# Kernel tuning notes

Hardware: AMD Instinct MI355X
Metric: run time of the kernel (lower is better)

The kernel has to match this reference:

```python
import jax, jax.numpy as jnp
import numpy as np

B, N, C = 4, 8192, 512
H, Dh, G, R = 8, 64, 64, 2  # heads, dim_head, slice_num, mlp_ratio
EPS_LN = 1e-5
EPS_NORM = 1e-5


def _ln(x, g, b):
    m = jnp.mean(x, axis=-1, keepdims=True)
    v = jnp.var(x, axis=-1, keepdims=True)
    return (x - m) * jax.lax.rsqrt(v + EPS_LN) * g + b


def setup_inputs() -> dict:
    key = jax.random.key(0)
    ks = jax.random.split(key, 16)
    r = lambda k, shp: jax.random.normal(k, shp, jnp.float32) * 0.02
    inner = H * Dh
    return {
        "fx": jax.random.normal(ks[0], (B, N, C), jnp.float32),
        "ln1_g": jnp.ones((C,), jnp.float32), "ln1_b": jnp.zeros((C,), jnp.float32),
        "Wx": r(ks[1], (C, inner)), "bx": jnp.zeros((inner,), jnp.float32),
        "Wfx": r(ks[2], (C, inner)), "bfx": jnp.zeros((inner,), jnp.float32),
        "Wslice": r(ks[3], (Dh, G)), "bslice": jnp.zeros((G,), jnp.float32),
        "temperature": jnp.full((1, H, 1, 1), 0.5, jnp.float32),
        "Wq": r(ks[4], (Dh, Dh)), "Wk": r(ks[5], (Dh, Dh)), "Wv": r(ks[6], (Dh, Dh)),
        "Wout": r(ks[7], (inner, C)), "bout": jnp.zeros((C,), jnp.float32),
        "tln_g": jnp.ones((Dh,), jnp.float32), "tln_b": jnp.zeros((Dh,), jnp.float32),
        "Wm1": r(ks[8], (Dh, R * Dh)), "bm1": jnp.zeros((R * Dh,), jnp.float32),
        "Wm2": r(ks[9], (R * Dh, Dh)), "bm2": jnp.zeros((Dh,), jnp.float32),
    }


def reference(fx, ln1_g, ln1_b, Wx, bx, Wfx, bfx, Wslice, bslice, temperature,
              Wq, Wk, Wv, Wout, bout, tln_g, tln_b, Wm1, bm1, Wm2, bm2):
    fx_norm = _ln(fx, ln1_g, ln1_b)                          # [B,N,C]
    # _forward_slice: project to per-head mid features
    x_mid = (fx_norm @ Wx + bx).reshape(B, N, H, Dh).transpose(0, 2, 1, 3)   # [B,H,N,Dh]
    fx_mid = (fx_norm @ Wfx + bfx).reshape(B, N, H, Dh).transpose(0, 2, 1, 3)
    # _project_token: soft slice assignment + weighted pooling into G tokens
    logits = jnp.einsum('bhnd,dg->bhng', x_mid, Wslice) + bslice
    slice_w = jax.nn.softmax(logits / temperature, axis=-1)  # [B,H,N,G]
    slice_norm = jnp.sum(slice_w, axis=2)                    # [B,H,G]
    slice_tok = jnp.einsum('bhnd,bhng->bhgd', fx_mid, slice_w) / (slice_norm[..., None] + EPS_NORM)
    # attention over the small token set (G tokens)
    q = slice_tok @ Wq
    k = slice_tok @ Wk
    v = slice_tok @ Wv
    scale = Dh ** -0.5
    attn = jax.nn.softmax(jnp.einsum('bhgd,bhpd->bhgp', q, k) * scale, axis=-1)
    out_tok = jnp.einsum('bhgp,bhpd->bhgd', attn, v) + slice_tok
    # token MLP with residual
    h = _ln(out_tok, tln_g, tln_b)
    h = jax.nn.gelu(h @ Wm1 + bm1, approximate=False) @ Wm2 + bm2
    tokens = h + out_tok                                     # [B,H,G,Dh]
    # _deslice: weighted scatter back to N points, merge heads, out projection
    out_x = jnp.einsum('bhgd,bhng->bhnd', tokens, slice_w)
    out_x = out_x.transpose(0, 2, 1, 3).reshape(B, N, H * Dh)
    out = out_x @ Wout + bout
    return out + fx_norm
```

## Files before the change

kernel.cpp:

```cpp
#include <hip/hip_runtime.h>
#include <math.h>

#define B_ 4
#define N_ 8192
#define C_ 512
#define H_ 8
#define M_ (B_ * N_)

typedef __attribute__((ext_vector_type(8))) short bf16x8;
typedef __attribute__((ext_vector_type(4))) float f32x4;
typedef __attribute__((ext_vector_type(8))) unsigned short u16x8;
typedef __attribute__((ext_vector_type(4))) unsigned short u16x4;

__device__ __forceinline__ float b2f(unsigned short u) {
  union { unsigned int i; float f; } v;
  v.i = ((unsigned int)u) << 16;
  return v.f;
}
__device__ __forceinline__ unsigned short f2b(float f) {
  union { float f; unsigned int i; } v;
  v.f = f;
  unsigned int r = v.i + 0x7fff + ((v.i >> 16) & 1);
  return (unsigned short)(r >> 16);
}
__device__ __forceinline__ void gl_lds16(const void* g, void* l) {
  __builtin_amdgcn_global_load_lds(
      (const __attribute__((address_space(1))) unsigned int*)g,
      (__attribute__((address_space(3))) unsigned int*)l, 16, 0, 0);
}

__global__ __launch_bounds__(256) void ln_bf16(
    const float* __restrict__ x, const float* __restrict__ gam,
    const float* __restrict__ bet, unsigned short* __restrict__ y) {
  int wave = threadIdx.x >> 6, lane = threadIdx.x & 63;
  int row = (blockIdx.x << 2) + wave;
  const float4* xr = (const float4*)(x + (size_t)row * C_);
  float4 v0 = xr[lane], v1 = xr[lane + 64];
  float s = v0.x + v0.y + v0.z + v0.w + v1.x + v1.y + v1.z + v1.w;
  float q = v0.x * v0.x + v0.y * v0.y + v0.z * v0.z + v0.w * v0.w +
            v1.x * v1.x + v1.y * v1.y + v1.z * v1.z + v1.w * v1.w;
#pragma unroll
  for (int off = 32; off; off >>= 1) {
    s += __shfl_xor(s, off);
    q += __shfl_xor(q, off);
  }
  float mean = s * (1.0f / C_);
  float var = q * (1.0f / C_) - mean * mean;
  float rstd = rsqrtf(var + 1e-5f);
  const float4* gr = (const float4*)gam;
  const float4* br = (const float4*)bet;
  float4 g0 = gr[lane], g1 = gr[lane + 64];
  float4 b0 = br[lane], b1 = br[lane + 64];
  u16x4 oa, ob;
  oa.x = f2b((v0.x - mean) * rstd * g0.x + b0.x);
  oa.y = f2b((v0.y - mean) * rstd * g0.y + b0.y);
  oa.z = f2b((v0.z - mean) * rstd * g0.z + b0.z);
  oa.w = f2b((v0.w - mean) * rstd * g0.w + b0.w);
  ob.x = f2b((v1.x - mean) * rstd * g1.x + b1.x);
  ob.y = f2b((v1.y - mean) * rstd * g1.y + b1.y);
  ob.z = f2b((v1.z - mean) * rstd * g1.z + b1.z);
  ob.w = f2b((v1.w - mean) * rstd * g1.w + b1.w);
  unsigned short* yr = y + (size_t)row * C_;
  *(u16x4*)(yr + (lane << 2)) = oa;
  *(u16x4*)(yr + 256 + (lane << 2)) = ob;
}

__global__ __launch_bounds__(256) void prep_all(
    const float* __restrict__ Wx, const float* __restrict__ Wfx,
    const float* __restrict__ Wout, const float* __restrict__ Wsl,
    const float* __restrict__ Wq, const float* __restrict__ Wk,
    const float* __restrict__ Wv, const float* __restrict__ Wm1,
    const float* __restrict__ Wm2, unsigned short* __restrict__ WtX,
    unsigned short* __restrict__ WtF, unsigned short* __restrict__ WtO,
    unsigned short* __restrict__ wsf, unsigned short* __restrict__ wfr) {
  __shared__ float tile[64][65];
  int blk = blockIdx.x, t = threadIdx.x;
  if (blk < 192) {
    int which = blk >> 6, sub = blk & 63;
    const float* W = (which == 0) ? Wx : (which == 1) ? Wfx : Wout;
    unsigned short* Wt = (which == 0) ? WtX : (which == 1) ? WtF : WtO;
    int r0 = (sub >> 3) << 6, c0 = (sub & 7) << 6;
    int lr = t >> 4, lc = (t & 15) << 2;
#pragma unroll
    for (int p = 0; p < 4; p++) {
      float4 v = *(const float4*)(W + (size_t)(r0 + lr + p * 16) * 512 + c0 + lc);
      tile[lr + p * 16][lc + 0] = v.x;
      tile[lr + p * 16][lc + 1] = v.y;
      tile[lr + p * 16][lc + 2] = v.z;
      tile[lr + p * 16][lc + 3] = v.w;
    }
    __syncthreads();
    int on = t >> 2, ok = (t & 3) << 4;
    unsigned short tmp[16];
#pragma unroll
    for (int j = 0; j < 16; j++) tmp[j] = f2b(tile[ok + j][on]);
    unsigned short* op = Wt + (size_t)(c0 + on) * 512 + r0 + ok;
#pragma unroll
    for (int j4 = 0; j4 < 4; j4++)
      *(u16x4*)(op + (j4 << 2)) = *(u16x4*)(tmp + (j4 << 2));
  } else {
#pragma unroll
    for (int i = 0; i < 2; i++) {
      int idx = t + i * 256;
      int f = idx >> 6, l = idx & 63;
      int gt = f >> 1, ks = f & 1;
      int g = (gt << 4) + (l & 15);
      int d0 = (ks << 5) + ((l >> 4) << 3);
      unsigned short v[8];
#pragma unroll
      for (int jj = 0; jj < 8; jj++) v[jj] = f2b(Wsl[(size_t)(d0 + jj) * 64 + g]);
      *(u16x4*)(wsf + idx * 8) = *(u16x4*)v;
      *(u16x4*)(wsf + idx * 8 + 4) = *(u16x4*)(v + 4);
    }
    for (int task = t; task < 56 * 64; task += 256) {
      int fid = task >> 6, l = task & 63;
      const float* W;
      int stride, ct, ks;
      if (fid < 24) {
        W = (fid < 8) ? Wq : (fid < 16) ? Wk : Wv;
        int e = fid & 7;
        ct = e >> 1;
        ks = e & 1;
        stride = 64;
      } else if (fid < 40) {
        W = Wm1;
        int e = fid - 24;
        ct = e >> 1;
        ks = e & 1;
        stride = 128;
      } else {
        W = Wm2;
        int e = fid - 40;
        ct = e >> 2;
        ks = e & 3;
        stride = 64;
      }
      int d0 = (ks << 5) + ((l >> 4) << 3);
      int c = (ct << 4) + (l & 15);
      unsigned short v[8];
#pragma unroll
      for (int j = 0; j < 8; j++) v[j] = f2b(W[(size_t)(d0 + j) * stride + c]);
      *(u16x4*)(wfr + task * 8) = *(u16x4*)v;
      *(u16x4*)(wfr + task * 8 + 4) = *(u16x4*)(v + 4);
    }
  }
}

__global__ __launch_bounds__(256) void tokfrag_prep(
    const float* __restrict__ tokens, unsigned short* __restrict__ wtokf) {
  int bh = blockIdx.x, t = threadIdx.x, w = t >> 6, l = t & 63;
  const float* tp = tokens + ((size_t)bh << 12);
#pragma unroll
  for (int fid = w; fid < 8; fid += 4) {
    int mt = fid >> 1, ks = fid & 1;
    int d = (mt << 4) + (l & 15);
    int g0 = (ks << 5) + ((l >> 4) << 3);
    unsigned short v[8];
#pragma unroll
    for (int j = 0; j < 8; j++) v[j] = f2b(tp[(g0 + j) * 64 + d]);
    unsigned short* op = wtokf + (((size_t)bh << 3) + fid) * 512 + (l << 3);
    *(u16x4*)op = *(u16x4*)v;
    *(u16x4*)(op + 4) = *(u16x4*)(v + 4);
  }
}

template <int DEC, bool BIASROW, bool OUTBF, bool RES>
__global__ __launch_bounds__(256) void gemm_bf16(
    const unsigned short* __restrict__ A, const unsigned short* __restrict__ Bt,
    const float* __restrict__ bias, const unsigned short* __restrict__ resid,
    void* __restrict__ Cout, size_t ldC) {
  __shared__ unsigned short lds[16384];
  const int t = threadIdx.x;
  const int w = t >> 6, l = t & 63;
  int bid = blockIdx.x;
  int xcd = bid & 7, q = bid >> 3;
  int bm, bn;
  if (DEC == 0) {
    bm = ((xcd << 5) + (q >> 2)) << 7;
    bn = (q & 3) << 7;
  } else {
    bn = ((xcd << 5) + (q >> 2)) << 7;
    bm = (q & 3) << 7;
  }
  const int wm = (w >> 1) << 6, wn = (w & 1) << 6;
  f32x4 acc[4][4];
#pragma unroll
  for (int mt = 0; mt < 4; mt++)
#pragma unroll
    for (int nt = 0; nt < 4; nt++) acc[mt][nt] = (f32x4){0.f, 0.f, 0.f, 0.f};

  const int srow = t >> 2;
  const int scol = (t & 3) << 3;
  const unsigned short* gA0 = A + (size_t)(bm + srow) * 512 + scol;
  const unsigned short* gA1 = A + (size_t)(bm + 64 + srow) * 512 + scol;
  const unsigned short* gB0 = Bt + (size_t)(bn + srow) * 512 + scol;
  const unsigned short* gB1 = Bt + (size_t)(bn + 64 + srow) * 512 + scol;
  const int fr = l & 15, fq = (l >> 4) << 3;

  gl_lds16(gA0, lds + (w << 9));
  gl_lds16(gA1, lds + 2048 + (w << 9));
  gl_lds16(gB0, lds + 4096 + (w << 9));
  gl_lds16(gB1, lds + 6144 + (w << 9));
  __syncthreads();
  int cur = 0;
  for (int ks = 0; ks < 16; ks++) {
    if (ks < 15) {
      int k0 = (ks + 1) << 5;
      unsigned short* st = lds + ((cur ^ 1) << 13);
      gl_lds16(gA0 + k0, st + (w << 9));
      gl_lds16(gA1 + k0, st + 2048 + (w << 9));
      gl_lds16(gB0 + k0, st + 4096 + (w << 9));
      gl_lds16(gB1 + k0, st + 6144 + (w << 9));
    }
    const unsigned short* lb = lds + (cur << 13);
    bf16x8 af[4], bfr[4];
#pragma unroll
    for (int mt = 0; mt < 4; mt++)
      af[mt] = *(const bf16x8*)&lb[(wm + mt * 16 + fr) * 32 + fq];
#pragma unroll
    for (int nt = 0; nt < 4; nt++)
      bfr[nt] = *(const bf16x8*)&lb[4096 + (wn + nt * 16 + fr) * 32 + fq];
#pragma unroll
    for (int mt = 0; mt < 4; mt++)
#pragma unroll
      for (int nt = 0; nt < 4; nt++)
        acc[mt][nt] = __builtin_amdgcn_mfma_f32_16x16x32_bf16(
            af[mt], bfr[nt], acc[mt][nt], 0, 0, 0);
    __syncthreads();
    cur ^= 1;
  }

  const int col0 = bn + wn + (l & 15);
  const int row0 = bm + wm + ((l >> 4) << 2);
#pragma unroll
  for (int mt = 0; mt < 4; mt++) {
#pragma unroll
    for (int j = 0; j < 4; j++) {
      int row = row0 + mt * 16 + j;
#pragma unroll
      for (int nt = 0; nt < 4; nt++) {
        int col = col0 + nt * 16;
        float v = acc[mt][nt][j] + (BIASROW ? bias[row] : bias[col]);
        if (RES) v += b2f(resid[(size_t)row * ldC + col]);
        if (OUTBF)
          ((unsigned short*)Cout)[(size_t)row * ldC + col] = f2b(v);
        else
          ((float*)Cout)[(size_t)row * ldC + col] = v;
      }
    }
  }
}

__global__ __launch_bounds__(256) void gemm_slice(
    const unsigned short* __restrict__ A, const unsigned short* __restrict__ Bt,
    const float* __restrict__ bias, const unsigned short* __restrict__ wf,
    const float* __restrict__ bslice, const float* __restrict__ temp,
    unsigned short* __restrict__ swout) {
  __shared__ unsigned short lds[16384];
  const int t = threadIdx.x;
  const int w = t >> 6, l = t & 63;
  int bid = blockIdx.x;
  int xcd = bid & 7, q = bid >> 3;
  const int bm = ((xcd << 5) + (q >> 2)) << 7;
  const int bn = (q & 3) << 7;
  const int wm = (w >> 1) << 6, wn = (w & 1) << 6;
  f32x4 acc[4][4];
#pragma unroll
  for (int mt = 0; mt < 4; mt++)
#pragma unroll
    for (int nt = 0; nt < 4; nt++) acc[mt][nt] = (f32x4){0.f, 0.f, 0.f, 0.f};

  const int srow = t >> 2;
  const int scol = (t & 3) << 3;
  const unsigned short* gA0 = A + (size_t)(bm + srow) * 512 + scol;
  const unsigned short* gA1 = A + (size_t)(bm + 64 + srow) * 512 + scol;
  const unsigned short* gB0 = Bt + (size_t)(bn + srow) * 512 + scol;
  const unsigned short* gB1 = Bt + (size_t)(bn + 64 + srow) * 512 + scol;
  const int fr = l & 15, fq = (l >> 4) << 3;

  gl_lds16(gA0, lds + (w << 9));
  gl_lds16(gA1, lds + 2048 + (w << 9));
  gl_lds16(gB0, lds + 4096 + (w << 9));
  gl_lds16(gB1, lds + 6144 + (w << 9));
  __syncthreads();
  int cur = 0;
  for (int ks = 0; ks < 16; ks++) {
    if (ks < 15) {
      int k0 = (ks + 1) << 5;
      unsigned short* st = lds + ((cur ^ 1) << 13);
      gl_lds16(gA0 + k0, st + (w << 9));
      gl_lds16(gA1 + k0, st + 2048 + (w << 9));
      gl_lds16(gB0 + k0, st + 4096 + (w << 9));
      gl_lds16(gB1 + k0, st + 6144 + (w << 9));
    }
    const unsigned short* lb = lds + (cur << 13);
    bf16x8 af[4], bfr[4];
#pragma unroll
    for (int mt = 0; mt < 4; mt++)
      af[mt] = *(const bf16x8*)&lb[(wm + mt * 16 + fr) * 32 + fq];
#pragma unroll
    for (int nt = 0; nt < 4; nt++)
      bfr[nt] = *(const bf16x8*)&lb[4096 + (wn + nt * 16 + fr) * 32 + fq];
#pragma unroll
    for (int mt = 0; mt < 4; mt++)
#pragma unroll
      for (int nt = 0; nt < 4; nt++)
        acc[mt][nt] = __builtin_amdgcn_mfma_f32_16x16x32_bf16(
            af[mt], bfr[nt], acc[mt][nt], 0, 0, 0);
    __syncthreads();
    cur ^= 1;
  }

  unsigned short* xt = lds + (w << 12);
  const int h = (bn + wn) >> 6;
  const int qq = l >> 4;
#pragma unroll
  for (int mt = 0; mt < 4; mt++)
#pragma unroll
    for (int nt = 0; nt < 4; nt++) {
      int d = (nt << 4) + fr;
      float bv = bias[bn + wn + d];
#pragma unroll
      for (int j = 0; j < 4; j++) {
        int r = (mt << 4) + (qq << 2) + j;
        xt[r * 64 + (((d >> 3) ^ (r & 7)) << 3) + (d & 7)] =
            f2b(acc[mt][nt][j] + bv);
      }
    }
  bf16x8 wsf[4][2];
#pragma unroll
  for (int gt = 0; gt < 4; gt++)
#pragma unroll
    for (int ks = 0; ks < 2; ks++)
      wsf[gt][ks] = *(const bf16x8*)(wf + (((gt << 1) + ks) * 64 + l) * 8);
  asm volatile("s_waitcnt lgkmcnt(0)" ::: "memory");
  __builtin_amdgcn_sched_barrier(0);

  float invt = 1.0f / temp[h];
#pragma unroll
  for (int rt = 0; rt < 4; rt++) {
    int xr = (rt << 4) + fr;
    f32x4 a4[4];
#pragma unroll
    for (int gt = 0; gt < 4; gt++) a4[gt] = (f32x4){0.f, 0.f, 0.f, 0.f};
#pragma unroll
    for (int ks = 0; ks < 2; ks++) {
      int slot = (ks << 2) + qq;
      bf16x8 xf = *(const bf16x8*)&xt[xr * 64 + ((slot ^ (xr & 7)) << 3)];
#pragma unroll
      for (int gt = 0; gt < 4; gt++)
        a4[gt] = __builtin_amdgcn_mfma_f32_16x16x32_bf16(wsf[gt][ks], xf,
                                                         a4[gt], 0, 0, 0);
    }
    float lg[16];
    float mx = -1e30f;
#pragma unroll
    for (int gt = 0; gt < 4; gt++)
#pragma unroll
      for (int r = 0; r < 4; r++) {
        float v = (a4[gt][r] + bslice[(gt << 4) + (qq << 2) + r]) * invt;
        lg[(gt << 2) + r] = v;
        mx = fmaxf(mx, v);
      }
    mx = fmaxf(mx, __shfl_xor(mx, 16));
    mx = fmaxf(mx, __shfl_xor(mx, 32));
    float ssum = 0.f;
#pragma unroll
    for (int i = 0; i < 16; i++) {
      lg[i] = expf(lg[i] - mx);
      ssum += lg[i];
    }
    ssum += __shfl_xor(ssum, 16);
    ssum += __shfl_xor(ssum, 32);
    float inv = 1.0f / ssum;
    asm volatile("s_waitcnt lgkmcnt(0)" ::: "memory");
#pragma unroll
    for (int gt = 0; gt < 4; gt++) {
      int slot = (gt << 1) + (qq >> 1);
      int off = ((slot ^ (xr & 7)) << 3) + ((qq & 1) << 2);
      u16x4 pk;
      pk.x = f2b(lg[(gt << 2) + 0] * inv);
      pk.y = f2b(lg[(gt << 2) + 1] * inv);
      pk.z = f2b(lg[(gt << 2) + 2] * inv);
      pk.w = f2b(lg[(gt << 2) + 3] * inv);
      *(u16x4*)&xt[xr * 64 + off] = pk;
    }
  }
  asm volatile("s_waitcnt lgkmcnt(0)" ::: "memory");
  __builtin_amdgcn_sched_barrier(0);
#pragma unroll
  for (int rt = 0; rt < 4; rt++) {
    int rr = (rt << 4) + (l >> 2);
    int sl = (l & 3) << 1, swz = rr & 7;
    u16x8 o0 = *(const u16x8*)&xt[rr * 64 + ((sl ^ swz) << 3)];
    u16x8 o1 = *(const u16x8*)&xt[rr * 64 + (((sl + 1) ^ swz) << 3)];
    unsigned short* op =
        swout + (size_t)(bm + wm + rr) * 512 + (h << 6) + ((l & 3) << 4);
    *(u16x8*)op = o0;
    *(u16x8*)(op + 8) = o1;
  }
}

__global__ __launch_bounds__(256) void pool_mfma(
    const unsigned short* __restrict__ sw, const unsigned short* __restrict__ fxT,
    float* __restrict__ tok_part, float* __restrict__ norm_part) {
  __shared__ unsigned short wT[4096];
  int bid = blockIdx.x;
  int bh = bid >> 4, c = bid & 15;
  int b = bh >> 3, h = bh & 7;
  int t = threadIdx.x, w = t >> 6, l = t & 63;
  int n0 = c << 9;
  const int fr15 = l & 15, fs = l >> 4;
  f32x4 acc[4];
#pragma unroll
  for (int gt = 0; gt < 4; gt++) acc[gt] = (f32x4){0.f, 0.f, 0.f, 0.f};
  float nacc[4] = {0.f, 0.f, 0.f, 0.f};

  const unsigned short* fxrow =
      fxT + (size_t)(h * 64 + w * 16 + fr15) * 32768 + b * N_ + n0 + (fs << 3);

  for (int nn = 0; nn < 512; nn += 64) {
    size_t srow = ((size_t)(b * N_ + n0 + nn + l) * 8 + h) << 6;
    u16x8 a0 = *(const u16x8*)(sw + srow + w * 16);
    u16x8 a1 = *(const u16x8*)(sw + srow + w * 16 + 8);
    __syncthreads();
#pragma unroll
    for (int j = 0; j < 16; j++) {
      int g = (w << 4) + j;
      unsigned short v = (j < 8) ? (unsigned short)a0[j] : (unsigned short)a1[j - 8];
      wT[(g << 6) + (((l >> 3) ^ (g & 7)) << 3) + (l & 7)] = v;
    }
    __syncthreads();
#pragma unroll
    for (int kk = 0; kk < 2; kk++) {
      bf16x8 bfrag = *(const bf16x8*)(fxrow + nn + (kk << 5));
#pragma unroll
      for (int gt = 0; gt < 4; gt++) {
        int g = (gt << 4) + fr15;
        int slot = (kk << 2) + fs;
        bf16x8 af = *(const bf16x8*)&wT[(g << 6) + ((slot ^ (g & 7)) << 3)];
        acc[gt] = __builtin_amdgcn_mfma_f32_16x16x32_bf16(af, bfrag, acc[gt], 0, 0, 0);
        if (w == 0) {
#pragma unroll
          for (int j = 0; j < 8; j++) nacc[gt] += b2f((unsigned short)af[j]);
        }
      }
    }
  }
  float* op = tok_part + ((size_t)bid << 12);
#pragma unroll
  for (int gt = 0; gt < 4; gt++)
#pragma unroll
    for (int rr = 0; rr < 4; rr++)
      op[((gt << 4) + (fs << 2) + rr) * 64 + (w << 4) + fr15] = acc[gt][rr];
  if (w == 0) {
#pragma unroll
    for (int gt = 0; gt < 4; gt++) {
      float s = nacc[gt];
      s += __shfl_xor(s, 16);
      s += __shfl_xor(s, 32);
      if (l < 16) norm_part[(bid << 6) + (gt << 4) + l] = s;
    }
  }
}

__global__ __launch_bounds__(256) void tok_reduce(
    const float* __restrict__ tok_part, const float* __restrict__ norm_part,
    float* __restrict__ stG) {
  int blk = blockIdx.x;
  int bh = blk >> 2, qq = blk & 3;
  int t = threadIdx.x;
  int e = (qq << 10) + (t << 2);
  int g = e >> 6;
  float s = 0.f;
  const float* np = norm_part + ((size_t)bh << 10);
#pragma unroll
  for (int c = 0; c < 16; c++) s += np[(c << 6) + g];
  float4 acc = make_float4(0.f, 0.f, 0.f, 0.f);
  const float* tp = tok_part + ((size_t)bh << 16) + e;
#pragma unroll
  for (int c = 0; c < 16; c++) {
    float4 v = *(const float4*)(tp + (c << 12));
    acc.x += v.x;
    acc.y += v.y;
    acc.z += v.z;
    acc.w += v.w;
  }
  float inv = 1.0f / (s + 1e-5f);
  acc.x *= inv;
  acc.y *= inv;
  acc.z *= inv;
  acc.w *= inv;
  *(float4*)(stG + ((size_t)bh << 12) + e) = acc;
}

__device__ __forceinline__ float gelu_exact(float x) {
  return 0.5f * x * (1.0f + erff(x * 0.70710678118654752f));
}

__global__ __launch_bounds__(256) void token_mfma(
    const float* __restrict__ stG, const unsigned short* __restrict__ wfr,
    const float* __restrict__ tg, const float* __restrict__ tb,
    const float* __restrict__ bm1, const float* __restrict__ bm2,
    float* __restrict__ tokens) {
  __shared__ __align__(16) char smem[54272];
  unsigned short* stb = (unsigned short*)smem;
  float* st32 = (float*)(smem + 9216);
  unsigned short* hmld = (unsigned short*)(smem + 9216);
  unsigned short* qld = (unsigned short*)(smem + 26624);
  unsigned short* kld = (unsigned short*)(smem + 35840);
  unsigned short* vtl = (unsigned short*)(smem + 45056);

  int bh = blockIdx.x, t = threadIdx.x, w = t >> 6, l = t & 63;
  const int fr = l & 15, fq = l >> 4;

  {
    int r = t >> 2, c0 = (t & 3) << 4;
    const float* gp = stG + ((size_t)bh << 12) + r * 64 + c0;
    float4 a = *(const float4*)gp;
    float4 b = *(const float4*)(gp + 4);
    float4 c = *(const float4*)(gp + 8);
    float4 d = *(const float4*)(gp + 12);
    *(float4*)&st32[r * 68 + c0] = a;
    *(float4*)&st32[r * 68 + c0 + 4] = b;
    *(float4*)&st32[r * 68 + c0 + 8] = c;
    *(float4*)&st32[r * 68 + c0 + 12] = d;
    unsigned short tv[16];
    tv[0] = f2b(a.x); tv[1] = f2b(a.y); tv[2] = f2b(a.z); tv[3] = f2b(a.w);
    tv[4] = f2b(b.x); tv[5] = f2b(b.y); tv[6] = f2b(b.z); tv[7] = f2b(b.w);
    tv[8] = f2b(c.x); tv[9] = f2b(c.y); tv[10] = f2b(c.z); tv[11] = f2b(c.w);
    tv[12] = f2b(d.x); tv[13] = f2b(d.y); tv[14] = f2b(d.z); tv[15] = f2b(d.w);
    *(u16x8*)&stb[r * 72 + c0] = *(u16x8*)tv;
    *(u16x8*)&stb[r * 72 + c0 + 8] = *(u16x8*)(tv + 8);
  }
  __syncthreads();

  const int orow = (w << 4) + (fq << 2);

  {
    bf16x8 af[2];
#pragma unroll
    for (int ks = 0; ks < 2; ks++)
      af[ks] = *(const bf16x8*)&stb[((w << 4) + fr) * 72 + (ks << 5) + (fq << 3)];
    f32x4 aq[4], ak[4], av[4];
#pragma unroll
    for (int ct = 0; ct < 4; ct++) {
      aq[ct] = (f32x4){0.f, 0.f, 0.f, 0.f};
      ak[ct] = (f32x4){0.f, 0.f, 0.f, 0.f};
      av[ct] = (f32x4){0.f, 0.f, 0.f, 0.f};
    }
#pragma unroll
    for (int ct = 0; ct < 4; ct++)
#pragma unroll
      for (int ks = 0; ks < 2; ks++) {
        bf16x8 bq = *(const bf16x8*)&wfr[(((ct << 1) + ks) * 64 + l) * 8];
        aq[ct] = __builtin_amdgcn_mfma_f32_16x16x32_bf16(af[ks], bq, aq[ct], 0, 0, 0);
      }
#pragma unroll
    for (int ct = 0; ct < 4; ct++)
#pragma unroll
      for (int ks = 0; ks < 2; ks++) {
        bf16x8 bk = *(const bf16x8*)&wfr[((8 + (ct << 1) + ks) * 64 + l) * 8];
        ak[ct] = __builtin_amdgcn_mfma_f32_16x16x32_bf16(af[ks], bk, ak[ct], 0, 0, 0);
      }
#pragma unroll
    for (int ct = 0; ct < 4; ct++)
#pragma unroll
      for (int ks = 0; ks < 2; ks++) {
        bf16x8 bv = *(const bf16x8*)&wfr[((16 + (ct << 1) + ks) * 64 + l) * 8];
        av[ct] = __builtin_amdgcn_mfma_f32_16x16x32_bf16(af[ks], bv, av[ct], 0, 0, 0);
      }
#pragma unroll
    for (int ct = 0; ct < 4; ct++) {
#pragma unroll
      for (int rr = 0; rr < 4; rr++) {
        qld[(orow + rr) * 72 + (ct << 4) + fr] = f2b(aq[ct][rr]);
        kld[(orow + rr) * 72 + (ct << 4) + fr] = f2b(ak[ct][rr]);
      }
      u16x4 vp;
      vp.x = f2b(av[ct][0]);
      vp.y = f2b(av[ct][1]);
      vp.z = f2b(av[ct][2]);
      vp.w = f2b(av[ct][3]);
      *(u16x4*)&vtl[((ct << 4) + fr) * 72 + orow] = vp;
    }
  }
  __syncthreads();

  {
    bf16x8 aq[2];
#pragma unroll
    for (int ks = 0; ks < 2; ks++)
      aq[ks] = *(const bf16x8*)&qld[((w << 4) + fr) * 72 + (ks << 5) + (fq << 3)];
    f32x4 accs[4];
#pragma unroll
    for (int nt = 0; nt < 4; nt++) accs[nt] = (f32x4){0.f, 0.f, 0.f, 0.f};
#pragma unroll
    for (int nt = 0; nt < 4; nt++)
#pragma unroll
      for (int ks = 0; ks < 2; ks++) {
        bf16x8 bk = *(const bf16x8*)&kld[((nt << 4) + fr) * 72 + (ks << 5) + (fq << 3)];
        accs[nt] = __builtin_amdgcn_mfma_f32_16x16x32_bf16(aq[ks], bk, accs[nt], 0, 0, 0);
      }
#pragma unroll
    for (int rr = 0; rr < 4; rr++) {
      float v0 = accs[0][rr] * 0.125f, v1 = accs[1][rr] * 0.125f;
      float v2 = accs[2][rr] * 0.125f, v3 = accs[3][rr] * 0.125f;
      float mx = fmaxf(fmaxf(v0, v1), fmaxf(v2, v3));
      mx = fmaxf(mx, __shfl_xor(mx, 1));
      mx = fmaxf(mx, __shfl_xor(mx, 2));
      mx = fmaxf(mx, __shfl_xor(mx, 4));
      mx = fmaxf(mx, __shfl_xor(mx, 8));
      float e0 = expf(v0 - mx), e1 = expf(v1 - mx);
      float e2 = expf(v2 - mx), e3 = expf(v3 - mx);
      float ss = e0 + e1 + e2 + e3;
      ss += __shfl_xor(ss, 1);
      ss += __shfl_xor(ss, 2);
      ss += __shfl_xor(ss, 4);
      ss += __shfl_xor(ss, 8);
      float inv = 1.0f / ss;
      stb[(orow + rr) * 72 + 0 * 16 + fr] = f2b(e0 * inv);
      stb[(orow + rr) * 72 + 1 * 16 + fr] = f2b(e1 * inv);
      stb[(orow + rr) * 72 + 2 * 16 + fr] = f2b(e2 * inv);
      stb[(orow + rr) * 72 + 3 * 16 + fr] = f2b(e3 * inv);
    }
  }
  __syncthreads();

  float o16[4][4];
  {
    bf16x8 ap[2];
#pragma unroll
    for (int ks = 0; ks < 2; ks++)
      ap[ks] = *(const bf16x8*)&stb[((w << 4) + fr) * 72 + (ks << 5) + (fq << 3)];
    f32x4 acco[4];
#pragma unroll
    for (int ct = 0; ct < 4; ct++) acco[ct] = (f32x4){0.f, 0.f, 0.f, 0.f};
#pragma unroll
    for (int ct = 0; ct < 4; ct++)
#pragma unroll
      for (int ks = 0; ks < 2; ks++) {
        bf16x8 bv = *(const bf16x8*)&vtl[((ct << 4) + fr) * 72 + (ks << 5) + (fq << 3)];
        acco[ct] = __builtin_amdgcn_mfma_f32_16x16x32_bf16(ap[ks], bv, acco[ct], 0, 0, 0);
      }
    float tgv[4], tbv[4];
#pragma unroll
    for (int ct = 0; ct < 4; ct++) {
      tgv[ct] = tg[(ct << 4) + fr];
      tbv[ct] = tb[(ct << 4) + fr];
    }
#pragma unroll
    for (int ct = 0; ct < 4; ct++)
#pragma unroll
      for (int rr = 0; rr < 4; rr++)
        o16[ct][rr] = acco[ct][rr] + st32[(orow + rr) * 68 + (ct << 4) + fr];
#pragma unroll
    for (int rr = 0; rr < 4; rr++) {
      float sm = o16[0][rr] + o16[1][rr] + o16[2][rr] + o16[3][rr];
      float sq = o16[0][rr] * o16[0][rr] + o16[1][rr] * o16[1][rr] +
                 o16[2][rr] * o16[2][rr] + o16[3][rr] * o16[3][rr];
      sm += __shfl_xor(sm, 1);
      sm += __shfl_xor(sm, 2);
      sm += __shfl_xor(sm, 4);
      sm += __shfl_xor(sm, 8);
      sq += __shfl_xor(sq, 1);
      sq += __shfl_xor(sq, 2);
      sq += __shfl_xor(sq, 4);
      sq += __shfl_xor(sq, 8);
      float mean = sm * (1.0f / 64.0f);
      float var = sq * (1.0f / 64.0f) - mean * mean;
      float rstd = rsqrtf(var + 1e-5f);
#pragma unroll
      for (int ct = 0; ct < 4; ct++) {
        float hv = (o16[ct][rr] - mean) * rstd * tgv[ct] + tbv[ct];
        qld[(orow + rr) * 72 + (ct << 4) + fr] = f2b(hv);
      }
    }
  }
  __syncthreads();

  {
    bf16x8 ah[2];
#pragma unroll
    for (int ks = 0; ks < 2; ks++)
      ah[ks] = *(const bf16x8*)&qld[((w << 4) + fr) * 72 + (ks << 5) + (fq << 3)];
    f32x4 accm[8];
#pragma unroll
    for (int et = 0; et < 8; et++) accm[et] = (f32x4){0.f, 0.f, 0.f, 0.f};
#pragma unroll
    for (int et = 0; et < 8; et++)
#pragma unroll
      for (int ks = 0; ks < 2; ks++) {
        bf16x8 bm = *(const bf16x8*)&wfr[((24 + (et << 1) + ks) * 64 + l) * 8];
        accm[et] = __builtin_amdgcn_mfma_f32_16x16x32_bf16(ah[ks], bm, accm[et], 0, 0, 0);
      }
#pragma unroll
    for (int et = 0; et < 8; et++) {
      float bv = bm1[(et << 4) + fr];
#pragma unroll
      for (int rr = 0; rr < 4; rr++) {
        float x = accm[et][rr] + bv;
        hmld[(orow + rr) * 136 + (et << 4) + fr] = f2b(gelu_exact(x));
      }
    }
  }
  __syncthreads();

  {
    bf16x8 ahm[4];
#pragma unroll
    for (int ks = 0; ks < 4; ks++)
      ahm[ks] = *(const bf16x8*)&hmld[((w << 4) + fr) * 136 + (ks << 5) + (fq << 3)];
    f32x4 acc2[4];
#pragma unroll
    for (int ct = 0; ct < 4; ct++) acc2[ct] = (f32x4){0.f, 0.f, 0.f, 0.f};
#pragma unroll
    for (int ct = 0; ct < 4; ct++)
#pragma unroll
      for (int ks = 0; ks < 4; ks++) {
        bf16x8 bw = *(const bf16x8*)&wfr[((40 + (ct << 2) + ks) * 64 + l) * 8];
        acc2[ct] = __builtin_amdgcn_mfma_f32_16x16x32_bf16(ahm[ks], bw, acc2[ct], 0, 0, 0);
      }
    float* tout = tokens + ((size_t)bh << 12);
#pragma unroll
    for (int ct = 0; ct < 4; ct++) {
      float bv = bm2[(ct << 4) + fr];
#pragma unroll
      for (int rr = 0; rr < 4; rr++)
        tout[(orow + rr) * 64 + (ct << 4) + fr] = acc2[ct][rr] + bv + o16[ct][rr];
    }
  }
}

__global__ __launch_bounds__(256) void deslice_mfma(
    const unsigned short* __restrict__ wtokf, const unsigned short* __restrict__ sw,
    unsigned short* __restrict__ outx) {
  int bid = blockIdx.x;
  int bh = bid >> 4, c = bid & 15;
  int b = bh >> 3, h = bh & 7;
  int t = threadIdx.x, w = t >> 6, l = t & 63;
  const int fr = l & 15, fq = l >> 4;

  bf16x8 ta[4][2];
  const unsigned short* fp = wtokf + ((size_t)bh << 12);
#pragma unroll
  for (int mt = 0; mt < 4; mt++)
#pragma unroll
    for (int ks = 0; ks < 2; ks++)
      ta[mt][ks] = *(const bf16x8*)(fp + (((mt << 1) + ks) << 9) + (l << 3));

  int n0 = (c << 9) + (w << 7);
#pragma unroll 2
  for (int ntile = 0; ntile < 8; ntile++) {
    int nb = n0 + (ntile << 4);
    size_t rowb = ((size_t)(b * N_ + nb + fr) * 8 + h) << 6;
    bf16x8 b0 = *(const bf16x8*)(sw + rowb + (fq << 3));
    bf16x8 b1 = *(const bf16x8*)(sw + rowb + 32 + (fq << 3));
    f32x4 acc[4];
#pragma unroll
    for (int mt = 0; mt < 4; mt++) acc[mt] = (f32x4){0.f, 0.f, 0.f, 0.f};
#pragma unroll
    for (int mt = 0; mt < 4; mt++) {
      acc[mt] = __builtin_amdgcn_mfma_f32_16x16x32_bf16(ta[mt][0], b0, acc[mt], 0, 0, 0);
      acc[mt] = __builtin_amdgcn_mfma_f32_16x16x32_bf16(ta[mt][1], b1, acc[mt], 0, 0, 0);
    }
    unsigned short* op = outx + rowb + (fq << 2);
#pragma unroll
    for (int mt = 0; mt < 4; mt++) {
      u16x4 pk;
      pk.x = f2b(acc[mt][0]);
      pk.y = f2b(acc[mt][1]);
      pk.z = f2b(acc[mt][2]);
      pk.w = f2b(acc[mt][3]);
      *(u16x4*)(op + (mt << 4)) = pk;
    }
  }
}

extern "C" void kernel_launch(void* const* d_in, const int* in_sizes, int n_in,
                              void* d_out, int out_size, void* d_ws,
                              size_t ws_size, hipStream_t stream) {
  const float* fx = (const float*)d_in[0];
  const float* ln1g = (const float*)d_in[1];
  const float* ln1b = (const float*)d_in[2];
  const float* Wx = (const float*)d_in[3];
  const float* bx = (const float*)d_in[4];
  const float* Wfx = (const float*)d_in[5];
  const float* bfx = (const float*)d_in[6];
  const float* Wsl = (const float*)d_in[7];
  const float* bsl = (const float*)d_in[8];
  const float* temp = (const float*)d_in[9];
  const float* Wq = (const float*)d_in[10];
  const float* Wk = (const float*)d_in[11];
  const float* Wv = (const float*)d_in[12];
  const float* Wout = (const float*)d_in[13];
  const float* bout = (const float*)d_in[14];
  const float* tlng = (const float*)d_in[15];
  const float* tlnb = (const float*)d_in[16];
  const float* Wm1 = (const float*)d_in[17];
  const float* bm1 = (const float*)d_in[18];
  const float* Wm2 = (const float*)d_in[19];
  const float* bm2 = (const float*)d_in[20];
  float* out = (float*)d_out;

  char* p = (char*)d_ws;
  const size_t MC2 = (size_t)M_ * 512 * 2;
  unsigned short* fxn = (unsigned short*)p;  p += MC2;
  unsigned short* buf1 = (unsigned short*)p; p += MC2;
  unsigned short* bufT = (unsigned short*)p; p += MC2;
  unsigned short* WtX = (unsigned short*)p;  p += 512 * 512 * 2;
  unsigned short* WtF = (unsigned short*)p;  p += 512 * 512 * 2;
  unsigned short* WtO = (unsigned short*)p;  p += 512 * 512 * 2;
  unsigned short* wsf = (unsigned short*)p;  p += 8192;
  unsigned short* wfr = (unsigned short*)p;  p += 56 * 512 * 2;
  unsigned short* wtokf = (unsigned short*)p; p += (size_t)32 * 8 * 512 * 2;
  float* tok_part = (float*)p;  p += (size_t)512 * 4096 * 4;
  float* norm_part = (float*)p; p += (size_t)512 * 64 * 4;
  float* tokens = (float*)p;    p += (size_t)32 * 4096 * 4;
  float* stG = (float*)p;       p += (size_t)32 * 4096 * 4;

  ln_bf16<<<M_ / 4, 256, 0, stream>>>(fx, ln1g, ln1b, fxn);
  prep_all<<<193, 256, 0, stream>>>(Wx, Wfx, Wout, Wsl, Wq, Wk, Wv, Wm1, Wm2,
                                    WtX, WtF, WtO, wsf, wfr);
  gemm_slice<<<1024, 256, 0, stream>>>(fxn, WtX, bx, wsf, bsl, temp, buf1);
  gemm_bf16<1, true, true, false><<<1024, 256, 0, stream>>>(WtF, fxn, bfx, nullptr, bufT, 32768);
  pool_mfma<<<512, 256, 0, stream>>>(buf1, bufT, tok_part, norm_part);
  tok_reduce<<<128, 256, 0, stream>>>(tok_part, norm_part, stG);
  token_mfma<<<32, 256, 0, stream>>>(stG, wfr, tlng, tlnb, bm1, bm2, tokens);
  tokfrag_prep<<<32, 256, 0, stream>>>(tokens, wtokf);
  deslice_mfma<<<512, 256, 0, stream>>>(wtokf, buf1, bufT);
  gemm_bf16<0, false, false, true><<<1024, 256, 0, stream>>>(bufT, WtO, bout, fxn, out, 512);
}
```

Before: 194.7 us.

## Halve GEMM LDS footprint: single-buffer, swizzled K-tiles, two-pass slice epilogue

Both bf16 GEMM kernels drop the double-buffered LDS pipeline in favor of a single 16KB buffer, loaded and consumed each K step between two barriers. The global-to-LDS source column is XOR-swizzled and the fragment read offset is matched, to cut LDS bank conflicts. The slice-softmax epilogue is split into two 32-row halves so each wave's scratch fits in the smaller buffer. The aim is to raise occupancy by using less LDS per block, at the cost of losing the overlap of global loads with MFMA work.

```diff
diff --git a/kernel.cpp b/kernel.cpp
--- a/kernel.cpp
+++ b/kernel.cpp
@@ -169,7 +169,7 @@
     const unsigned short* __restrict__ A, const unsigned short* __restrict__ Bt,
     const float* __restrict__ bias, const unsigned short* __restrict__ resid,
     void* __restrict__ Cout, size_t ldC) {
-  __shared__ unsigned short lds[16384];
+  __shared__ unsigned short lds[8192];
   const int t = threadIdx.x;
   const int w = t >> 6, l = t & 63;
   int bid = blockIdx.x;
@@ -190,36 +190,27 @@
     for (int nt = 0; nt < 4; nt++) acc[mt][nt] = (f32x4){0.f, 0.f, 0.f, 0.f};
 
   const int srow = t >> 2;
-  const int scol = (t & 3) << 3;
+  const int scol = (((t & 3) ^ ((t >> 3) & 3)) << 3);
   const unsigned short* gA0 = A + (size_t)(bm + srow) * 512 + scol;
   const unsigned short* gA1 = A + (size_t)(bm + 64 + srow) * 512 + scol;
   const unsigned short* gB0 = Bt + (size_t)(bn + srow) * 512 + scol;
   const unsigned short* gB1 = Bt + (size_t)(bn + 64 + srow) * 512 + scol;
-  const int fr = l & 15, fq = (l >> 4) << 3;
-
-  gl_lds16(gA0, lds + (w << 9));
-  gl_lds16(gA1, lds + 2048 + (w << 9));
-  gl_lds16(gB0, lds + 4096 + (w << 9));
-  gl_lds16(gB1, lds + 6144 + (w << 9));
-  __syncthreads();
-  int cur = 0;
-  for (int ks = 0; ks < 16; ks++) {
-    if (ks < 15) {
-      int k0 = (ks + 1) << 5;
-      unsigned short* st = lds + ((cur ^ 1) << 13);
-      gl_lds16(gA0 + k0, st + (w << 9));
-      gl_lds16(gA1 + k0, st + 2048 + (w << 9));
-      gl_lds16(gB0 + k0, st + 4096 + (w << 9));
-      gl_lds16(gB1 + k0, st + 6144 + (w << 9));
-    }
-    const unsigned short* lb = lds + (cur << 13);
+  const int fr = l & 15;
+  const int pslot = (((l >> 4) ^ ((l >> 1) & 3)) << 3);
+
+  for (int k0 = 0; k0 < 512; k0 += 32) {
+    gl_lds16(gA0 + k0, lds + (w << 9));
+    gl_lds16(gA1 + k0, lds + 2048 + (w << 9));
+    gl_lds16(gB0 + k0, lds + 4096 + (w << 9));
+    gl_lds16(gB1 + k0, lds + 6144 + (w << 9));
+    __syncthreads();
     bf16x8 af[4], bfr[4];
 #pragma unroll
     for (int mt = 0; mt < 4; mt++)
-      af[mt] = *(const bf16x8*)&lb[(wm + mt * 16 + fr) * 32 + fq];
+      af[mt] = *(const bf16x8*)&lds[(wm + mt * 16 + fr) * 32 + pslot];
 #pragma unroll
     for (int nt = 0; nt < 4; nt++)
-      bfr[nt] = *(const bf16x8*)&lb[4096 + (wn + nt * 16 + fr) * 32 + fq];
+      bfr[nt] = *(const bf16x8*)&lds[4096 + (wn + nt * 16 + fr) * 32 + pslot];
 #pragma unroll
     for (int mt = 0; mt < 4; mt++)
 #pragma unroll
@@ -227,7 +218,6 @@
         acc[mt][nt] = __builtin_amdgcn_mfma_f32_16x16x32_bf16(
             af[mt], bfr[nt], acc[mt][nt], 0, 0, 0);
     __syncthreads();
-    cur ^= 1;
   }
 
   const int col0 = bn + wn + (l & 15);
@@ -256,7 +246,7 @@
     const float* __restrict__ bias, const unsigned short* __restrict__ wf,
     const float* __restrict__ bslice, const float* __restrict__ temp,
     unsigned short* __restrict__ swout) {
-  __shared__ unsigned short lds[16384];
+  __shared__ unsigned short lds[8192];
   const int t = threadIdx.x;
   const int w = t >> 6, l = t & 63;
   int bid = blockIdx.x;
@@ -271,36 +261,27 @@
     for (int nt = 0; nt < 4; nt++) acc[mt][nt] = (f32x4){0.f, 0.f, 0.f, 0.f};
 
   const int srow = t >> 2;
-  const int scol = (t & 3) << 3;
+  const int scol = (((t & 3) ^ ((t >> 3) & 3)) << 3);
   const unsigned short* gA0 = A + (size_t)(bm + srow) * 512 + scol;
   const unsigned short* gA1 = A + (size_t)(bm + 64 + srow) * 512 + scol;
   const unsigned short* gB0 = Bt + (size_t)(bn + srow) * 512 + scol;
   const unsigned short* gB1 = Bt + (size_t)(bn + 64 + srow) * 512 + scol;
-  const int fr = l & 15, fq = (l >> 4) << 3;
-
-  gl_lds16(gA0, lds + (w << 9));
-  gl_lds16(gA1, lds + 2048 + (w << 9));
-  gl_lds16(gB0, lds + 4096 + (w << 9));
-  gl_lds16(gB1, lds + 6144 + (w << 9));
-  __syncthreads();
-  int cur = 0;
-  for (int ks = 0; ks < 16; ks++) {
-    if (ks < 15) {
-      int k0 = (ks + 1) << 5;
-      unsigned short* st = lds + ((cur ^ 1) << 13);
-      gl_lds16(gA0 + k0, st + (w << 9));
-      gl_lds16(gA1 + k0, st + 2048 + (w << 9));
-      gl_lds16(gB0 + k0, st + 4096 + (w << 9));
-      gl_lds16(gB1 + k0, st + 6144 + (w << 9));
-    }
-    const unsigned short* lb = lds + (cur << 13);
+  const int fr = l & 15;
+  const int pslot = (((l >> 4) ^ ((l >> 1) & 3)) << 3);
+
+  for (int k0 = 0; k0 < 512; k0 += 32) {
+    gl_lds16(gA0 + k0, lds + (w << 9));
+    gl_lds16(gA1 + k0, lds + 2048 + (w << 9));
+    gl_lds16(gB0 + k0, lds + 4096 + (w << 9));
+    gl_lds16(gB1 + k0, lds + 6144 + (w << 9));
+    __syncthreads();
     bf16x8 af[4], bfr[4];
 #pragma unroll
     for (int mt = 0; mt < 4; mt++)
-      af[mt] = *(const bf16x8*)&lb[(wm + mt * 16 + fr) * 32 + fq];
+      af[mt] = *(const bf16x8*)&lds[(wm + mt * 16 + fr) * 32 + pslot];
 #pragma unroll
     for (int nt = 0; nt < 4; nt++)
-      bfr[nt] = *(const bf16x8*)&lb[4096 + (wn + nt * 16 + fr) * 32 + fq];
+      bfr[nt] = *(const bf16x8*)&lds[4096 + (wn + nt * 16 + fr) * 32 + pslot];
 #pragma unroll
     for (int mt = 0; mt < 4; mt++)
 #pragma unroll
@@ -308,96 +289,100 @@
         acc[mt][nt] = __builtin_amdgcn_mfma_f32_16x16x32_bf16(
             af[mt], bfr[nt], acc[mt][nt], 0, 0, 0);
     __syncthreads();
-    cur ^= 1;
-  }
-
-  unsigned short* xt = lds + (w << 12);
+  }
+
+  unsigned short* xt = lds + (w << 11);
   const int h = (bn + wn) >> 6;
   const int qq = l >> 4;
-#pragma unroll
-  for (int mt = 0; mt < 4; mt++)
-#pragma unroll
-    for (int nt = 0; nt < 4; nt++) {
-      int d = (nt << 4) + fr;
-      float bv = bias[bn + wn + d];
-#pragma unroll
-      for (int j = 0; j < 4; j++) {
-        int r = (mt << 4) + (qq << 2) + j;
-        xt[r * 64 + (((d >> 3) ^ (r & 7)) << 3) + (d & 7)] =
-            f2b(acc[mt][nt][j] + bv);
-      }
-    }
+  float invt = 1.0f / temp[h];
   bf16x8 wsf[4][2];
 #pragma unroll
   for (int gt = 0; gt < 4; gt++)
 #pragma unroll
     for (int ks = 0; ks < 2; ks++)
       wsf[gt][ks] = *(const bf16x8*)(wf + (((gt << 1) + ks) * 64 + l) * 8);
-  asm volatile("s_waitcnt lgkmcnt(0)" ::: "memory");
-  __builtin_amdgcn_sched_barrier(0);
-
-  float invt = 1.0f / temp[h];
-#pragma unroll
-  for (int rt = 0; rt < 4; rt++) {
-    int xr = (rt << 4) + fr;
-    f32x4 a4[4];
-#pragma unroll
-    for (int gt = 0; gt < 4; gt++) a4[gt] = (f32x4){0.f, 0.f, 0.f, 0.f};
-#pragma unroll
-    for (int ks = 0; ks < 2; ks++) {
-      int slot = (ks << 2) + qq;
-      bf16x8 xf = *(const bf16x8*)&xt[xr * 64 + ((slot ^ (xr & 7)) << 3)];
+
+#pragma unroll
+  for (int hh = 0; hh < 2; hh++) {
+    asm volatile("s_waitcnt lgkmcnt(0)" ::: "memory");
+    __builtin_amdgcn_sched_barrier(0);
+#pragma unroll
+    for (int mt = 0; mt < 2; mt++)
+#pragma unroll
+      for (int nt = 0; nt < 4; nt++) {
+        int d = (nt << 4) + fr;
+        float bv = bias[bn + wn + d];
+#pragma unroll
+        for (int j = 0; j < 4; j++) {
+          int r = (mt << 4) + (qq << 2) + j;
+          xt[r * 64 + (((d >> 3) ^ (r & 7)) << 3) + (d & 7)] =
+              f2b(acc[(hh << 1) + mt][nt][j] + bv);
+        }
+      }
+    asm volatile("s_waitcnt lgkmcnt(0)" ::: "memory");
+    __builtin_amdgcn_sched_barrier(0);
+#pragma unroll
+    for (int rt = 0; rt < 2; rt++) {
+      int xr = (rt << 4) + fr;
+      f32x4 a4[4];
+#pragma unroll
+      for (int gt = 0; gt < 4; gt++) a4[gt] = (f32x4){0.f, 0.f, 0.f, 0.f};
+#pragma unroll
+      for (int ks = 0; ks < 2; ks++) {
+        int slot = (ks << 2) + qq;
+        bf16x8 xf = *(const bf16x8*)&xt[xr * 64 + ((slot ^ (xr & 7)) << 3)];
+#pragma unroll
+        for (int gt = 0; gt < 4; gt++)
+          a4[gt] = __builtin_amdgcn_mfma_f32_16x16x32_bf16(wsf[gt][ks], xf,
+                                                           a4[gt], 0, 0, 0);
+      }
+      float lg[16];
+      float mx = -1e30f;
 #pragma unroll
       for (int gt = 0; gt < 4; gt++)
-        a4[gt] = __builtin_amdgcn_mfma_f32_16x16x32_bf16(wsf[gt][ks], xf,
-                                                         a4[gt], 0, 0, 0);
-    }
-    float lg[16];
-    float mx = -1e30f;
-#pragma unroll
-    for (int gt = 0; gt < 4; gt++)
-#pragma unroll
-      for (int r = 0; r < 4; r++) {
-        float v = (a4[gt][r] + bslice[(gt << 4) + (qq << 2) + r]) * invt;
-        lg[(gt << 2) + r] = v;
-        mx = fmaxf(mx, v);
-      }
-    mx = fmaxf(mx, __shfl_xor(mx, 16));
-    mx = fmaxf(mx, __shfl_xor(mx, 32));
-    float ssum = 0.f;
-#pragma unroll
-    for (int i = 0; i < 16; i++) {
-      lg[i] = expf(lg[i] - mx);
-      ssum += lg[i];
-    }
-    ssum += __shfl_xor(ssum, 16);
-    ssum += __shfl_xor(ssum, 32);
-    float inv = 1.0f / ssum;
+#pragma unroll
+        for (int r = 0; r < 4; r++) {
+          float v = (a4[gt][r] + bslice[(gt << 4) + (qq << 2) + r]) * invt;
+          lg[(gt << 2) + r] = v;
+          mx = fmaxf(mx, v);
+        }
+      mx = fmaxf(mx, __shfl_xor(mx, 16));
+      mx = fmaxf(mx, __shfl_xor(mx, 32));
+      float ssum = 0.f;
+#pragma unroll
+      for (int i = 0; i < 16; i++) {
+        lg[i] = expf(lg[i] - mx);
+        ssum += lg[i];
+      }
+      ssum += __shfl_xor(ssum, 16);
+      ssum += __shfl_xor(ssum, 32);
+      float inv = 1.0f / ssum;
+      asm volatile("s_waitcnt lgkmcnt(0)" ::: "memory");
+#pragma unroll
+      for (int gt = 0; gt < 4; gt++) {
+        int slot = (gt << 1) + (qq >> 1);
+        int off = ((slot ^ (xr & 7)) << 3) + ((qq & 1) << 2);
+        u16x4 pk;
+        pk.x = f2b(lg[(gt << 2) + 0] * inv);
+        pk.y = f2b(lg[(gt << 2) + 1] * inv);
+        pk.z = f2b(lg[(gt << 2) + 2] * inv);
+        pk.w = f2b(lg[(gt << 2) + 3] * inv);
+        *(u16x4*)&xt[xr * 64 + off] = pk;
+      }
+    }
     asm volatile("s_waitcnt lgkmcnt(0)" ::: "memory");
-#pragma unroll
-    for (int gt = 0; gt < 4; gt++) {
-      int slot = (gt << 1) + (qq >> 1);
-      int off = ((slot ^ (xr & 7)) << 3) + ((qq & 1) << 2);
-      u16x4 pk;
-      pk.x = f2b(lg[(gt << 2) + 0] * inv);
-      pk.y = f2b(lg[(gt << 2) + 1] * inv);
-      pk.z = f2b(lg[(gt << 2) + 2] * inv);
-      pk.w = f2b(lg[(gt << 2) + 3] * inv);
-      *(u16x4*)&xt[xr * 64 + off] = pk;
-    }
-  }
-  asm volatile("s_waitcnt lgkmcnt(0)" ::: "memory");
-  __builtin_amdgcn_sched_barrier(0);
-#pragma unroll
-  for (int rt = 0; rt < 4; rt++) {
-    int rr = (rt << 4) + (l >> 2);
-    int sl = (l & 3) << 1, swz = rr & 7;
-    u16x8 o0 = *(const u16x8*)&xt[rr * 64 + ((sl ^ swz) << 3)];
-    u16x8 o1 = *(const u16x8*)&xt[rr * 64 + (((sl + 1) ^ swz) << 3)];
-    unsigned short* op =
-        swout + (size_t)(bm + wm + rr) * 512 + (h << 6) + ((l & 3) << 4);
-    *(u16x8*)op = o0;
-    *(u16x8*)(op + 8) = o1;
+    __builtin_amdgcn_sched_barrier(0);
+#pragma unroll
+    for (int rt = 0; rt < 2; rt++) {
+      int rr = (rt << 4) + (l >> 2);
+      int sl = (l & 3) << 1, swz = rr & 7;
+      u16x8 o0 = *(const u16x8*)&xt[rr * 64 + ((sl ^ swz) << 3)];
+      u16x8 o1 = *(const u16x8*)&xt[rr * 64 + (((sl + 1) ^ swz) << 3)];
+      unsigned short* op = swout + (size_t)(bm + wm + (hh << 5) + rr) * 512 +
+                           (h << 6) + ((l & 3) << 4);
+      *(u16x8*)op = o0;
+      *(u16x8*)(op + 8) = o1;
+    }
   }
 }
 
```

After: 180.9 us. -7.1%, faster.
